# Kernel tuning notes

Hardware: AMD Instinct MI355X
Metric: run time of the kernel (lower is better)

## Reference

```python
import jax, jax.numpy as jnp
import numpy as np

EMBED_SIZE = 1024
HEADS = 16
HEAD_DIM = EMBED_SIZE // HEADS  # 64


def setup_inputs() -> dict:
    key = jax.random.key(0)
    k_x, k_q, k_k, k_v, k_o, k_b = jax.random.split(key, 6)
    B, S = 32, 8192  # S divisible by HEADS
    x = jax.random.normal(k_x, (B, S, HEAD_DIM), dtype=jnp.float32)
    # torch.nn.Linear weights are [out, in]; scale ~ 1/sqrt(fan_in)
    s_h = 1.0 / np.sqrt(HEAD_DIM)
    s_e = 1.0 / np.sqrt(EMBED_SIZE)
    Wq = jax.random.uniform(k_q, (HEAD_DIM, HEAD_DIM), jnp.float32, -s_h, s_h)
    Wk = jax.random.uniform(k_k, (HEAD_DIM, HEAD_DIM), jnp.float32, -s_h, s_h)
    Wv = jax.random.uniform(k_v, (HEAD_DIM, HEAD_DIM), jnp.float32, -s_h, s_h)
    Wo = jax.random.uniform(k_o, (EMBED_SIZE, EMBED_SIZE), jnp.float32, -s_e, s_e)
    bo = jax.random.uniform(k_b, (EMBED_SIZE,), jnp.float32, -s_e, s_e)
    return {"x": x, "Wq": Wq, "Wk": Wk, "Wv": Wv, "Wo": Wo, "bo": bo}


def reference(x, Wq, Wk, Wv, Wo, bo):
    B = x.shape[0]
    # Q/K/V projections: Linear(head_dim, head_dim), bias=False -> x @ W.T
    Q = (x @ Wq.T).reshape(B, -1, HEADS, HEAD_DIM)  # [B, G, H, D], G = S/H
    K = (x @ Wk.T).reshape(B, -1, HEADS, HEAD_DIM)
    V = (x @ Wv.T).reshape(B, -1, HEADS, HEAD_DIM)
    # energy = Q @ K^T over last two dims -> [B, G, H, H]
    energy = jnp.einsum('bghd,bgkd->bghk', Q, K)
    attn = jax.nn.softmax(energy / jnp.sqrt(jnp.float32(EMBED_SIZE)), axis=3)
    out = jnp.einsum('bghk,bgkd->bghd', attn, V)      # [B, G, H, D]
    out = out.transpose(0, 2, 1, 3).reshape(B, -1, EMBED_SIZE)  # [B, S/H, E]
    return out @ Wo.T + bo
```

## Files before the change

### kernel.cpp

```cpp
#include <hip/hip_runtime.h>
#include <hip/hip_bf16.h>
#include <stdint.h>

#define TOKS   262144
#define NGRP   16384
#define EMB    1024
#define HD     64

using bf16x8 = __attribute__((ext_vector_type(8))) short;
using f32x4  = __attribute__((ext_vector_type(4))) float;

__device__ __forceinline__ unsigned pack2(float a, float b) {
    union { __hip_bfloat162 h; unsigned u; } cvt;
    cvt.h = __float22bfloat162_rn(make_float2(a, b));
    return cvt.u;
}
__device__ __forceinline__ bf16x8 cvt8(float4 v0, float4 v1) {
    uint4 u;
    u.x = pack2(v0.x, v0.y);
    u.y = pack2(v0.z, v0.w);
    u.z = pack2(v1.x, v1.y);
    u.w = pack2(v1.z, v1.w);
    return __builtin_bit_cast(bf16x8, u);
}

__global__ __launch_bounds__(256) void k_cvt(const float* __restrict__ wo,
                                             const float* __restrict__ wq,
                                             const float* __restrict__ wk,
                                             const float* __restrict__ wv,
                                             unsigned short* __restrict__ wob,
                                             unsigned short* __restrict__ wqkvb) {
    int bid = blockIdx.x;
    if (bid < 512) {
        int tid = bid * 256 + threadIdx.x;
        int kc  = tid >> 12;
        int nb  = (tid >> 6) & 63;
        int l   = tid & 63;
        int n   = nb * 16 + (l & 15);
        int k   = kc * 32 + (l >> 4) * 8;
        const float* src = wo + (size_t)n * 1024 + k;
        float4 v0 = *(const float4*)(src);
        float4 v1 = *(const float4*)(src + 4);
        *(bf16x8*)(wob + (size_t)tid * 8) = cvt8(v0, v1);
    } else {
        int b = bid - 512;
        int m = b >> 2;
        const float* src = (m == 0) ? wq : ((m == 1) ? wk : wv);
        int idx = ((b & 3) * 256 + threadIdx.x) * 4;
        float4 v = *(const float4*)(src + idx);
        uint2 p;
        p.x = pack2(v.x, v.y);
        p.y = pack2(v.z, v.w);
        *(uint2*)(wqkvb + m * 4096 + idx) = p;
    }
}

#define SCL 0.0450842200278f

#define MFMA_B16(A, B, Cc) __builtin_amdgcn_mfma_f32_16x16x32_bf16(A, B, Cc, 0, 0, 0)

__global__ __launch_bounds__(512, 2) void k_mega(const float* __restrict__ x,
                                                 const unsigned short* __restrict__ wqkv,
                                                 const unsigned short* __restrict__ wob,
                                                 const float* __restrict__ bias,
                                                 float* __restrict__ C) {
    extern __shared__ __align__(16) unsigned short lds[];
    unsigned short* out2s = lds;
    unsigned short* kscr  = lds + 65536;

    const int t = threadIdx.x;
    const int w = t >> 6, l = t & 63;
    const int c = l & 15, q = l >> 4;
    const int bid   = blockIdx.x;
    const int batch = bid >> 3, q8 = bid & 7;
    unsigned short* kw = kscr + w * 1024;

    #pragma unroll 1
    for (int i = 0; i < 8; ++i) {
        const int gl   = w * 8 + i;
        const int gbq  = gl >> 4;
        const int gcol = gl & 15;
        const size_t tok0 = (size_t)bid * 1024 + (size_t)gl * 16;

        bf16x8 xa[2];
        {
            const float* xp = x + (tok0 + c) * 64 + q * 8;
            #pragma unroll
            for (int kc = 0; kc < 2; ++kc) {
                float4 v0 = *(const float4*)(xp + kc * 32);
                float4 v1 = *(const float4*)(xp + kc * 32 + 4);
                xa[kc] = cvt8(v0, v1);
            }
        }

        const int mQ0 = gbq << 3;
        const int mQ1 = 32 + (gbq << 3);
        unsigned short* qslot = out2s + (size_t)(16 * q + gbq) * 1024 + gcol * 64;

        uint2 pkV[4];
        #pragma unroll
        for (int m = 0; m < 3; ++m) {
            #pragma unroll
            for (int nb = 0; nb < 4; ++nb) {
                const unsigned short* wp = wqkv + m * 4096 + (nb * 16 + c) * 64 + q * 8;
                bf16x8 w0 = *(const bf16x8*)(wp);
                bf16x8 w1 = *(const bf16x8*)(wp + 32);
                f32x4 acc = (f32x4){0.f, 0.f, 0.f, 0.f};
                acc = MFMA_B16(xa[0], w0, acc);
                acc = MFMA_B16(xa[1], w1, acc);
                unsigned u01 = pack2(acc[0], acc[1]);
                unsigned u23 = pack2(acc[2], acc[3]);
                const int d = nb * 16 + c;
                if (m == 0) {
                    qslot[(d ^ mQ0)]              = (unsigned short)u01;
                    qslot[4 * 1024 + (d ^ mQ1)]   = (unsigned short)(u01 >> 16);
                    qslot[8 * 1024 + (d ^ mQ0)]   = (unsigned short)u23;
                    qslot[12 * 1024 + (d ^ mQ1)]  = (unsigned short)(u23 >> 16);
                } else if (m == 1) {
                    const int kr = 4 * q;
                    kw[(kr + 0) * 64 + (d ^ (((kr + 0) & 7) << 3))] = (unsigned short)u01;
                    kw[(kr + 1) * 64 + (d ^ (((kr + 1) & 7) << 3))] = (unsigned short)(u01 >> 16);
                    kw[(kr + 2) * 64 + (d ^ (((kr + 2) & 7) << 3))] = (unsigned short)u23;
                    kw[(kr + 3) * 64 + (d ^ (((kr + 3) & 7) << 3))] = (unsigned short)(u23 >> 16);
                } else {
                    pkV[nb].x = u01;
                    pkV[nb].y = u23;
                }
            }
        }

        f32x4 e = (f32x4){0.f, 0.f, 0.f, 0.f};
        {
            const int mq = ((c * 4 + gbq) & 7) << 3;
            const unsigned short* qrow = out2s + (size_t)(c * 4 + gbq) * 1024 + gcol * 64;
            #pragma unroll
            for (int kc = 0; kc < 2; ++kc) {
                const int L = kc * 32 + q * 8;
                bf16x8 ka = *(const bf16x8*)(kw + c * 64 + (L ^ ((c & 7) << 3)));
                bf16x8 qb = *(const bf16x8*)(qrow + (L ^ mq));
                e = MFMA_B16(ka, qb, e);
            }
        }

        unsigned pa0, pa1;
        {
            float mx = fmaxf(fmaxf(e[0], e[1]), fmaxf(e[2], e[3]));
            mx = fmaxf(mx, __shfl_xor(mx, 16));
            mx = fmaxf(mx, __shfl_xor(mx, 32));
            float p0 = exp2f((e[0] - mx) * SCL);
            float p1 = exp2f((e[1] - mx) * SCL);
            float p2 = exp2f((e[2] - mx) * SCL);
            float p3 = exp2f((e[3] - mx) * SCL);
            float s = p0 + p1 + p2 + p3;
            s += __shfl_xor(s, 16);
            s += __shfl_xor(s, 32);
            float rinv = 1.0f / s;
            pa0 = pack2(p0 * rinv, p1 * rinv);
            pa1 = pack2(p2 * rinv, p3 * rinv);
        }

        {
            const int sh0 = (32 * q + c) & 63;
            const int sh1 = (32 * q + 16 + c) & 63;
            const int sv0 = 32 * (q & 1) + c;
            const int sv1 = sv0 + 16;
            const bool hi = (q >= 2);
            int a0 = __shfl((int)pa0, sh0);
            int a1 = __shfl((int)pa1, sh0);
            int a2 = __shfl((int)pa0, sh1);
            int a3 = __shfl((int)pa1, sh1);
            uint4 A2u;
            A2u.x = hi ? 0u : (unsigned)a0;
            A2u.y = hi ? 0u : (unsigned)a1;
            A2u.z = hi ? 0u : (unsigned)a2;
            A2u.w = hi ? 0u : (unsigned)a3;
            bf16x8 A2 = __builtin_bit_cast(bf16x8, A2u);

            #pragma unroll
            for (int nb = 0; nb < 4; ++nb) {
                uint4 B2u;
                B2u.x = (unsigned)__shfl((int)pkV[nb].x, sv0);
                B2u.y = (unsigned)__shfl((int)pkV[nb].y, sv0);
                B2u.z = (unsigned)__shfl((int)pkV[nb].x, sv1);
                B2u.w = (unsigned)__shfl((int)pkV[nb].y, sv1);
                bf16x8 B2 = __builtin_bit_cast(bf16x8, B2u);
                f32x4 o = (f32x4){0.f, 0.f, 0.f, 0.f};
                o = MFMA_B16(A2, B2, o);
                unsigned u01 = pack2(o[0], o[1]);
                unsigned u23 = pack2(o[2], o[3]);
                const int d = nb * 16 + c;
                qslot[(d ^ mQ0)]              = (unsigned short)u01;
                qslot[4 * 1024 + (d ^ mQ1)]   = (unsigned short)(u01 >> 16);
                qslot[8 * 1024 + (d ^ mQ0)]   = (unsigned short)u23;
                qslot[12 * 1024 + (d ^ mQ1)]  = (unsigned short)(u23 >> 16);
            }
        }
    }

    __syncthreads();

    const unsigned short* gBw = wob + (size_t)(w * 8) * 512 + (size_t)l * 8;
    float bc[8];
    #pragma unroll
    for (int nb = 0; nb < 8; ++nb) bc[nb] = bias[w * 128 + nb * 16 + c];

    f32x4 acc[4][8];
    #pragma unroll
    for (int m = 0; m < 4; ++m)
        #pragma unroll
        for (int nb = 0; nb < 8; ++nb)
            acc[m][nb] = (f32x4){0.f, 0.f, 0.f, 0.f};

    const int axor = (c & 7) << 3;
    bf16x8 bE[8], bO[8], a[4];

    #pragma unroll
    for (int nb = 0; nb < 8; ++nb) bE[nb] = *(const bf16x8*)(gBw + nb * 512);

    #pragma unroll 1
    for (int tt = 0; tt < 16; ++tt) {
        const size_t kb = (size_t)tt * 65536;
        #pragma unroll
        for (int nb = 0; nb < 8; ++nb)
            bO[nb] = *(const bf16x8*)(gBw + kb + 32768 + nb * 512);
        {
            const int L = (2 * tt) * 32 + q * 8;
            #pragma unroll
            for (int m = 0; m < 4; ++m)
                a[m] = *(const bf16x8*)(out2s + (size_t)(m * 16 + c) * 1024 + (L ^ axor));
            #pragma unroll
            for (int m = 0; m < 4; ++m)
                #pragma unroll
                for (int nb = 0; nb < 8; ++nb)
                    acc[m][nb] = MFMA_B16(a[m], bE[nb], acc[m][nb]);
        }
        if (tt < 15) {
            #pragma unroll
            for (int nb = 0; nb < 8; ++nb)
                bE[nb] = *(const bf16x8*)(gBw + kb + 65536 + nb * 512);
        }
        {
            const int L = (2 * tt + 1) * 32 + q * 8;
            #pragma unroll
            for (int m = 0; m < 4; ++m)
                a[m] = *(const bf16x8*)(out2s + (size_t)(m * 16 + c) * 1024 + (L ^ axor));
            #pragma unroll
            for (int m = 0; m < 4; ++m)
                #pragma unroll
                for (int nb = 0; nb < 8; ++nb)
                    acc[m][nb] = MFMA_B16(a[m], bO[nb], acc[m][nb]);
        }
    }

    #pragma unroll
    for (int m = 0; m < 4; ++m) {
        #pragma unroll
        for (int r = 0; r < 4; ++r) {
            const int rg = batch * 512 + (m * 4 + q) * 32 + q8 * 4 + r;
            float* cp = C + (size_t)rg * 1024 + w * 128 + c;
            #pragma unroll
            for (int nb = 0; nb < 8; ++nb)
                cp[nb * 16] = acc[m][nb][r] + bc[nb];
        }
    }
}

extern "C" void kernel_launch(void* const* d_in, const int* in_sizes, int n_in,
                              void* d_out, int out_size, void* d_ws, size_t ws_size,
                              hipStream_t stream) {
    const float* x  = (const float*)d_in[0];
    const float* wq = (const float*)d_in[1];
    const float* wk = (const float*)d_in[2];
    const float* wv = (const float*)d_in[3];
    const float* wo = (const float*)d_in[4];
    const float* bo = (const float*)d_in[5];
    float* out = (float*)d_out;

    unsigned short* wob   = (unsigned short*)d_ws;
    unsigned short* wqkvb = wob + (size_t)EMB * EMB;

    static int s_once = []() {
        hipFuncSetAttribute((const void*)k_mega,
                            hipFuncAttributeMaxDynamicSharedMemorySize, 147456);
        return 0;
    }();
    (void)s_once;

    k_cvt <<<524, 256, 0, stream>>>(wo, wq, wk, wv, wob, wqkvb);
    k_mega<<<256, 512, 147456, stream>>>(x, wqkvb, wob, bo, out);
}
```

Baseline: 151.4 us.

## Process two groups per iteration, prefetch x, and use a stronger LDS swizzle

Restructures the attention phase so each wave handles two 16-token groups per iteration, sharing the bf16 weight fragment loads across both and prefetching the next pair of x tiles into registers while the current pair computes. The LDS XOR swizzle is replaced with a function that mixes more row bits, meant to reduce bank conflicts in the scattered Q/out stores and the later A-fragment reads. The group-to-wave mapping is changed to match. This raises register pressure, which could hurt occupancy at 512 threads with two blocks per CU.

```diff
diff --git a/kernel.cpp b/kernel.cpp
--- a/kernel.cpp
+++ b/kernel.cpp
@@ -22,6 +22,9 @@
     u.z = pack2(v1.x, v1.y);
     u.w = pack2(v1.z, v1.w);
     return __builtin_bit_cast(bf16x8, u);
+}
+__device__ __forceinline__ int swz(int r) {
+    return ((r ^ (r >> 2) ^ (r >> 4)) & 7) << 3;
 }
 
 __global__ __launch_bounds__(256) void k_cvt(const float* __restrict__ wo,
@@ -72,103 +75,155 @@
     const int w = t >> 6, l = t & 63;
     const int c = l & 15, q = l >> 4;
     const int bid   = blockIdx.x;
-    const int batch = bid >> 3, q8 = bid & 7;
+    const int batch = bid >> 3, q8 = bid & 3 + 0, q8r = bid & 7;
     unsigned short* kw = kscr + w * 1024;
 
+    const int gbq = w >> 1;
+    const int gc0 = (w & 1) * 8;
+
+    const int mS0 = swz(16 * q + gbq);
+    const int mS1 = swz(16 * q + gbq + 4);
+    const int mS2 = swz(16 * q + gbq + 8);
+    const int mS3 = swz(16 * q + gbq + 12);
+    const int mkw = swz(c);
+    const int mqe = swz(c * 4 + gbq);
+    const int mk0 = swz(4 * q);
+    const int mk1 = swz(4 * q + 1);
+    const int mk2 = swz(4 * q + 2);
+    const int mk3 = swz(4 * q + 3);
+
+    const float* xb = x + ((size_t)bid * 1024 + c) * 64 + q * 8;
+
+    float4 xr[2][4];
+    #pragma unroll
+    for (int g = 0; g < 2; ++g) {
+        const float* xp = xb + (size_t)(w * 8 + g) * 1024;
+        xr[g][0] = *(const float4*)(xp);
+        xr[g][1] = *(const float4*)(xp + 4);
+        xr[g][2] = *(const float4*)(xp + 32);
+        xr[g][3] = *(const float4*)(xp + 36);
+    }
+
     #pragma unroll 1
-    for (int i = 0; i < 8; ++i) {
-        const int gl   = w * 8 + i;
-        const int gbq  = gl >> 4;
-        const int gcol = gl & 15;
-        const size_t tok0 = (size_t)bid * 1024 + (size_t)gl * 16;
-
-        bf16x8 xa[2];
-        {
-            const float* xp = x + (tok0 + c) * 64 + q * 8;
-            #pragma unroll
-            for (int kc = 0; kc < 2; ++kc) {
-                float4 v0 = *(const float4*)(xp + kc * 32);
-                float4 v1 = *(const float4*)(xp + kc * 32 + 4);
-                xa[kc] = cvt8(v0, v1);
-            }
-        }
-
-        const int mQ0 = gbq << 3;
-        const int mQ1 = 32 + (gbq << 3);
-        unsigned short* qslot = out2s + (size_t)(16 * q + gbq) * 1024 + gcol * 64;
-
-        uint2 pkV[4];
-        #pragma unroll
-        for (int m = 0; m < 3; ++m) {
+    for (int p = 0; p < 4; ++p) {
+        bf16x8 xa[2][2];
+        #pragma unroll
+        for (int g = 0; g < 2; ++g) {
+            xa[g][0] = cvt8(xr[g][0], xr[g][1]);
+            xa[g][1] = cvt8(xr[g][2], xr[g][3]);
+        }
+        if (p < 3) {
+            #pragma unroll
+            for (int g = 0; g < 2; ++g) {
+                const float* xp = xb + (size_t)(w * 8 + 2 * (p + 1) + g) * 1024;
+                xr[g][0] = *(const float4*)(xp);
+                xr[g][1] = *(const float4*)(xp + 4);
+                xr[g][2] = *(const float4*)(xp + 32);
+                xr[g][3] = *(const float4*)(xp + 36);
+            }
+        }
+
+        unsigned short* qs[2];
+        qs[0] = out2s + (size_t)(16 * q + gbq) * 1024 + (gc0 + 2 * p) * 64;
+        qs[1] = qs[0] + 64;
+
+        #pragma unroll
+        for (int nb = 0; nb < 4; ++nb) {
+            const unsigned short* wp = wqkv + (nb * 16 + c) * 64 + q * 8;
+            bf16x8 w0 = *(const bf16x8*)(wp);
+            bf16x8 w1 = *(const bf16x8*)(wp + 32);
+            #pragma unroll
+            for (int g = 0; g < 2; ++g) {
+                f32x4 acc = (f32x4){0.f, 0.f, 0.f, 0.f};
+                acc = MFMA_B16(xa[g][0], w0, acc);
+                acc = MFMA_B16(xa[g][1], w1, acc);
+                unsigned u01 = pack2(acc[0], acc[1]);
+                unsigned u23 = pack2(acc[2], acc[3]);
+                const int d = nb * 16 + c;
+                qs[g][(d ^ mS0)]             = (unsigned short)u01;
+                qs[g][4 * 1024 + (d ^ mS1)]  = (unsigned short)(u01 >> 16);
+                qs[g][8 * 1024 + (d ^ mS2)]  = (unsigned short)u23;
+                qs[g][12 * 1024 + (d ^ mS3)] = (unsigned short)(u23 >> 16);
+            }
+        }
+
+        uint2 pkV[2][4];
+        #pragma unroll
+        for (int nb = 0; nb < 4; ++nb) {
+            const unsigned short* wp = wqkv + 2 * 4096 + (nb * 16 + c) * 64 + q * 8;
+            bf16x8 w0 = *(const bf16x8*)(wp);
+            bf16x8 w1 = *(const bf16x8*)(wp + 32);
+            #pragma unroll
+            for (int g = 0; g < 2; ++g) {
+                f32x4 acc = (f32x4){0.f, 0.f, 0.f, 0.f};
+                acc = MFMA_B16(xa[g][0], w0, acc);
+                acc = MFMA_B16(xa[g][1], w1, acc);
+                pkV[g][nb].x = pack2(acc[0], acc[1]);
+                pkV[g][nb].y = pack2(acc[2], acc[3]);
+            }
+        }
+
+        f32x4 e[2];
+        #pragma unroll
+        for (int g = 0; g < 2; ++g) {
             #pragma unroll
             for (int nb = 0; nb < 4; ++nb) {
-                const unsigned short* wp = wqkv + m * 4096 + (nb * 16 + c) * 64 + q * 8;
+                const unsigned short* wp = wqkv + 4096 + (nb * 16 + c) * 64 + q * 8;
                 bf16x8 w0 = *(const bf16x8*)(wp);
                 bf16x8 w1 = *(const bf16x8*)(wp + 32);
                 f32x4 acc = (f32x4){0.f, 0.f, 0.f, 0.f};
-                acc = MFMA_B16(xa[0], w0, acc);
-                acc = MFMA_B16(xa[1], w1, acc);
+                acc = MFMA_B16(xa[g][0], w0, acc);
+                acc = MFMA_B16(xa[g][1], w1, acc);
                 unsigned u01 = pack2(acc[0], acc[1]);
                 unsigned u23 = pack2(acc[2], acc[3]);
                 const int d = nb * 16 + c;
-                if (m == 0) {
-                    qslot[(d ^ mQ0)]              = (unsigned short)u01;
-                    qslot[4 * 1024 + (d ^ mQ1)]   = (unsigned short)(u01 >> 16);
-                    qslot[8 * 1024 + (d ^ mQ0)]   = (unsigned short)u23;
-                    qslot[12 * 1024 + (d ^ mQ1)]  = (unsigned short)(u23 >> 16);
-                } else if (m == 1) {
-                    const int kr = 4 * q;
-                    kw[(kr + 0) * 64 + (d ^ (((kr + 0) & 7) << 3))] = (unsigned short)u01;
-                    kw[(kr + 1) * 64 + (d ^ (((kr + 1) & 7) << 3))] = (unsigned short)(u01 >> 16);
-                    kw[(kr + 2) * 64 + (d ^ (((kr + 2) & 7) << 3))] = (unsigned short)u23;
-                    kw[(kr + 3) * 64 + (d ^ (((kr + 3) & 7) << 3))] = (unsigned short)(u23 >> 16);
-                } else {
-                    pkV[nb].x = u01;
-                    pkV[nb].y = u23;
-                }
-            }
-        }
-
-        f32x4 e = (f32x4){0.f, 0.f, 0.f, 0.f};
-        {
-            const int mq = ((c * 4 + gbq) & 7) << 3;
-            const unsigned short* qrow = out2s + (size_t)(c * 4 + gbq) * 1024 + gcol * 64;
-            #pragma unroll
-            for (int kc = 0; kc < 2; ++kc) {
-                const int L = kc * 32 + q * 8;
-                bf16x8 ka = *(const bf16x8*)(kw + c * 64 + (L ^ ((c & 7) << 3)));
-                bf16x8 qb = *(const bf16x8*)(qrow + (L ^ mq));
-                e = MFMA_B16(ka, qb, e);
-            }
-        }
-
-        unsigned pa0, pa1;
-        {
-            float mx = fmaxf(fmaxf(e[0], e[1]), fmaxf(e[2], e[3]));
+                const int kr = 4 * q;
+                kw[(kr + 0) * 64 + (d ^ mk0)] = (unsigned short)u01;
+                kw[(kr + 1) * 64 + (d ^ mk1)] = (unsigned short)(u01 >> 16);
+                kw[(kr + 2) * 64 + (d ^ mk2)] = (unsigned short)u23;
+                kw[(kr + 3) * 64 + (d ^ mk3)] = (unsigned short)(u23 >> 16);
+            }
+            e[g] = (f32x4){0.f, 0.f, 0.f, 0.f};
+            const unsigned short* qrow = out2s + (size_t)(c * 4 + gbq) * 1024
+                                               + (gc0 + 2 * p + g) * 64;
+            #pragma unroll
+            for (int kc2 = 0; kc2 < 2; ++kc2) {
+                const int L = kc2 * 32 + q * 8;
+                bf16x8 ka = *(const bf16x8*)(kw + c * 64 + (L ^ mkw));
+                bf16x8 qb = *(const bf16x8*)(qrow + (L ^ mqe));
+                e[g] = MFMA_B16(ka, qb, e[g]);
+            }
+        }
+
+        unsigned pa0[2], pa1[2];
+        #pragma unroll
+        for (int g = 0; g < 2; ++g) {
+            float mx = fmaxf(fmaxf(e[g][0], e[g][1]), fmaxf(e[g][2], e[g][3]));
             mx = fmaxf(mx, __shfl_xor(mx, 16));
             mx = fmaxf(mx, __shfl_xor(mx, 32));
-            float p0 = exp2f((e[0] - mx) * SCL);
-            float p1 = exp2f((e[1] - mx) * SCL);
-            float p2 = exp2f((e[2] - mx) * SCL);
-            float p3 = exp2f((e[3] - mx) * SCL);
+            float p0 = exp2f((e[g][0] - mx) * SCL);
+            float p1 = exp2f((e[g][1] - mx) * SCL);
+            float p2 = exp2f((e[g][2] - mx) * SCL);
+            float p3 = exp2f((e[g][3] - mx) * SCL);
             float s = p0 + p1 + p2 + p3;
             s += __shfl_xor(s, 16);
             s += __shfl_xor(s, 32);
             float rinv = 1.0f / s;
-            pa0 = pack2(p0 * rinv, p1 * rinv);
-            pa1 = pack2(p2 * rinv, p3 * rinv);
-        }
-
-        {
-            const int sh0 = (32 * q + c) & 63;
-            const int sh1 = (32 * q + 16 + c) & 63;
-            const int sv0 = 32 * (q & 1) + c;
-            const int sv1 = sv0 + 16;
-            const bool hi = (q >= 2);
-            int a0 = __shfl((int)pa0, sh0);
-            int a1 = __shfl((int)pa1, sh0);
-            int a2 = __shfl((int)pa0, sh1);
-            int a3 = __shfl((int)pa1, sh1);
+            pa0[g] = pack2(p0 * rinv, p1 * rinv);
+            pa1[g] = pack2(p2 * rinv, p3 * rinv);
+        }
+
+        const int sh0 = (32 * q + c) & 63;
+        const int sh1 = (32 * q + 16 + c) & 63;
+        const int sv0 = 32 * (q & 1) + c;
+        const int sv1 = sv0 + 16;
+        const bool hi = (q >= 2);
+        #pragma unroll
+        for (int g = 0; g < 2; ++g) {
+            int a0 = __shfl((int)pa0[g], sh0);
+            int a1 = __shfl((int)pa1[g], sh0);
+            int a2 = __shfl((int)pa0[g], sh1);
+            int a3 = __shfl((int)pa1[g], sh1);
             uint4 A2u;
             A2u.x = hi ? 0u : (unsigned)a0;
             A2u.y = hi ? 0u : (unsigned)a1;
@@ -179,20 +234,20 @@
             #pragma unroll
             for (int nb = 0; nb < 4; ++nb) {
                 uint4 B2u;
-                B2u.x = (unsigned)__shfl((int)pkV[nb].x, sv0);
-                B2u.y = (unsigned)__shfl((int)pkV[nb].y, sv0);
-                B2u.z = (unsigned)__shfl((int)pkV[nb].x, sv1);
-                B2u.w = (unsigned)__shfl((int)pkV[nb].y, sv1);
+                B2u.x = (unsigned)__shfl((int)pkV[g][nb].x, sv0);
+                B2u.y = (unsigned)__shfl((int)pkV[g][nb].y, sv0);
+                B2u.z = (unsigned)__shfl((int)pkV[g][nb].x, sv1);
+                B2u.w = (unsigned)__shfl((int)pkV[g][nb].y, sv1);
                 bf16x8 B2 = __builtin_bit_cast(bf16x8, B2u);
                 f32x4 o = (f32x4){0.f, 0.f, 0.f, 0.f};
                 o = MFMA_B16(A2, B2, o);
                 unsigned u01 = pack2(o[0], o[1]);
                 unsigned u23 = pack2(o[2], o[3]);
                 const int d = nb * 16 + c;
-                qslot[(d ^ mQ0)]              = (unsigned short)u01;
-                qslot[4 * 1024 + (d ^ mQ1)]   = (unsigned short)(u01 >> 16);
-                qslot[8 * 1024 + (d ^ mQ0)]   = (unsigned short)u23;
-                qslot[12 * 1024 + (d ^ mQ1)]  = (unsigned short)(u23 >> 16);
+                qs[g][(d ^ mS0)]             = (unsigned short)u01;
+                qs[g][4 * 1024 + (d ^ mS1)]  = (unsigned short)(u01 >> 16);
+                qs[g][8 * 1024 + (d ^ mS2)]  = (unsigned short)u23;
+                qs[g][12 * 1024 + (d ^ mS3)] = (unsigned short)(u23 >> 16);
             }
         }
     }
@@ -211,7 +266,6 @@
         for (int nb = 0; nb < 8; ++nb)
             acc[m][nb] = (f32x4){0.f, 0.f, 0.f, 0.f};
 
-    const int axor = (c & 7) << 3;
     bf16x8 bE[8], bO[8], a[4];
 
     #pragma unroll
@@ -227,7 +281,8 @@
             const int L = (2 * tt) * 32 + q * 8;
             #pragma unroll
             for (int m = 0; m < 4; ++m)
-                a[m] = *(const bf16x8*)(out2s + (size_t)(m * 16 + c) * 1024 + (L ^ axor));
+                a[m] = *(const bf16x8*)(out2s + (size_t)(m * 16 + c) * 1024
+                                              + (L ^ swz(m * 16 + c)));
             #pragma unroll
             for (int m = 0; m < 4; ++m)
                 #pragma unroll
@@ -243,7 +298,8 @@
             const int L = (2 * tt + 1) * 32 + q * 8;
             #pragma unroll
             for (int m = 0; m < 4; ++m)
-                a[m] = *(const bf16x8*)(out2s + (size_t)(m * 16 + c) * 1024 + (L ^ axor));
+                a[m] = *(const bf16x8*)(out2s + (size_t)(m * 16 + c) * 1024
+                                              + (L ^ swz(m * 16 + c)));
             #pragma unroll
             for (int m = 0; m < 4; ++m)
                 #pragma unroll
@@ -256,7 +312,7 @@
     for (int m = 0; m < 4; ++m) {
         #pragma unroll
         for (int r = 0; r < 4; ++r) {
-            const int rg = batch * 512 + (m * 4 + q) * 32 + q8 * 4 + r;
+            const int rg = batch * 512 + (m * 4 + q) * 32 + q8r * 4 + r;
             float* cp = C + (size_t)rg * 1024 + w * 128 + c;
             #pragma unroll
             for (int nb = 0; nb < 8; ++nb)
```

Measured after the change: 151.5 us. No clear change (+0.0%).
